# Kernel tuning notes

Measured on AMD Instinct MI355X. Metric: run time of the kernel, lower is better.

The kernel has to match this reference:

```python
import jax, jax.numpy as jnp
import numpy as np

TOTAL_WORDS = 90000
EMBED = 100
SEQ = 300
BATCH = 250
UNITS = 1024


def setup_inputs() -> dict:
    key = jax.random.key(0)
    ks = jax.random.split(key, 9)
    s = 0.02
    return {
        "tokens": jax.random.randint(ks[0], (BATCH, SEQ), 0, TOTAL_WORDS),
        "emb": jax.random.normal(ks[1], (TOTAL_WORDS, EMBED), jnp.float32) * s,
        "Wx0": jax.random.normal(ks[2], (EMBED, UNITS), jnp.float32) * s,
        "Wh0": jax.random.normal(ks[3], (UNITS, UNITS), jnp.float32) * s,
        "b0": jnp.zeros((UNITS,), jnp.float32),
        "Wx1": jax.random.normal(ks[4], (UNITS, UNITS), jnp.float32) * s,
        "Wh1": jax.random.normal(ks[5], (UNITS, UNITS), jnp.float32) * s,
        "b1": jnp.zeros((UNITS,), jnp.float32),
        "Wo": jax.random.normal(ks[6], (UNITS, 1), jnp.float32) * s,
        "bo": jnp.zeros((1,), jnp.float32),
    }


def reference(tokens, emb, Wx0, Wh0, b0, Wx1, Wh1, b1, Wo, bo):
    # Embedding lookup: [B, S, E]
    x = emb[tokens]
    # Precompute input projections for both cells' input-side matmuls where possible.
    # Cell0 input projection can be done for all timesteps at once: [B, S, U]
    xp0 = jnp.einsum("bse,eu->bsu", x, Wx0) + b0

    def step(carry, xp_t):
        h0, h1 = carry
        # SimpleRNNCell: out = tanh(x@Wx + h@Wh + b); dropout disabled (inference)
        h0 = jnp.tanh(xp_t + h0 @ Wh0)
        h1 = jnp.tanh(h0 @ Wx1 + h1 @ Wh1 + b1)
        return (h0, h1), None

    h0 = jnp.zeros((BATCH, UNITS), jnp.float32)
    h1 = jnp.zeros((BATCH, UNITS), jnp.float32)
    # scan over time: xp0 transposed to [S, B, U]
    (h0, h1), _ = jax.lax.scan(step, (h0, h1), jnp.transpose(xp0, (1, 0, 2)))
    logits = h1 @ Wo + bo  # [B, 1]
    return jax.nn.sigmoid(logits)
```

## Files before the change

kernel.cpp:

```cpp
#include <hip/hip_runtime.h>
#include <hip/hip_bf16.h>

#define SEQ 300
#define BAT 250
#define UNITS 1024
#define EMBD 100
#define MROWS (SEQ*BAT)

typedef __bf16 bf16;
typedef __bf16 bf16x4 __attribute__((ext_vector_type(4)));
typedef __bf16 bf16x8 __attribute__((ext_vector_type(8)));
typedef float  f32x2  __attribute__((ext_vector_type(2)));
typedef float  f32x4  __attribute__((ext_vector_type(4)));
typedef float  f32x16 __attribute__((ext_vector_type(16)));
typedef unsigned u32x4 __attribute__((ext_vector_type(4)));

#define MFMA32(a,b,c) __builtin_amdgcn_mfma_f32_32x32x16_bf16(a,b,c,0,0,0)
#define F32X16_ZERO {0.f,0.f,0.f,0.f,0.f,0.f,0.f,0.f,0.f,0.f,0.f,0.f,0.f,0.f,0.f,0.f}

__device__ __align__(16)  bf16 g_xp0[(size_t)MROWS*UNITS + 8192];
__device__ __align__(256) bf16 g_h0[304][256*1024];
__device__ __align__(256) bf16 g_h1[304][256*1024];
__device__ __align__(64) unsigned g_pf0[8*16];
__device__ __align__(64) unsigned g_pf1[8*16];

struct L16 { u32x4 a, b, c, d; };

#define ISSUE_LINE(L, P) \
  asm volatile("global_load_dwordx4 %0, %4, off sc0 sc1\n\t" \
               "global_load_dwordx4 %1, %4, off offset:16 sc0 sc1\n\t" \
               "global_load_dwordx4 %2, %4, off offset:32 sc0 sc1\n\t" \
               "global_load_dwordx4 %3, %4, off offset:48 sc0 sc1" \
    : "=&v"((L).a), "=&v"((L).b), "=&v"((L).c), "=&v"((L).d) : "v"(P) : "memory")
#define ISSUE8(A, B, P) \
  asm volatile("global_load_dwordx4 %0, %2, off sc0 sc1\n\t" \
               "global_load_dwordx4 %1, %2, off offset:16 sc0 sc1" \
    : "=&v"(A), "=&v"(B) : "v"(P) : "memory")

__device__ __forceinline__ unsigned min8(const u32x4& a, const u32x4& b) {
  unsigned m0 = a[0] < a[1] ? a[0] : a[1];
  unsigned m1 = a[2] < a[3] ? a[2] : a[3];
  unsigned m2 = b[0] < b[1] ? b[0] : b[1];
  unsigned m3 = b[2] < b[3] ? b[2] : b[3];
  m0 = m0 < m1 ? m0 : m1; m2 = m2 < m3 ? m2 : m3;
  return m0 < m2 ? m0 : m2;
}
__device__ __forceinline__ unsigned minline(const L16& L) {
  unsigned m0 = min8(L.a, L.b), m1 = min8(L.c, L.d);
  return m0 < m1 ? m0 : m1;
}
__device__ __forceinline__ float tanh_fast(float x) {
  float e = __expf(2.f * x);
  return 1.f - 2.f / (e + 1.f);
}

__global__ __launch_bounds__(256) void xp0_kernel(const int* __restrict__ tokens,
                                                  const float* __restrict__ emb,
                                                  const float* __restrict__ Wx0,
                                                  const float* __restrict__ b0) {
  __shared__ bf16 A[64 * 128];
  __shared__ int toks[64];
  const int mt = blockIdx.x;
  const int nt = blockIdx.y;
  const int tid = threadIdx.x, lane = tid & 63, wv = tid >> 6;

  if (tid < 64) {
    int R = mt * 64 + tid;
    int tok = 0;
    if (R < MROWS) { int s = R / 250; int b = R - s * 250; tok = tokens[b * SEQ + s]; }
    toks[tid] = tok;
  }
  __syncthreads();
  for (int idx = tid; idx < 64 * 128; idx += 256) {
    int r = idx >> 7, k = idx & 127;
    float v = (k < EMBD) ? emb[(size_t)toks[r] * EMBD + k] : 0.f;
    unsigned off = (unsigned)(r * 256 + k * 2);
    off ^= (unsigned)((r & 7) << 4);
    *(bf16*)((char*)A + off) = (bf16)v;
  }

  const int colb = nt * 256 + (wv << 6) + (lane & 31);
  bf16x8 Bf[2][8];
  #pragma unroll
  for (int nf = 0; nf < 2; ++nf) {
    #pragma unroll
    for (int kk = 0; kk < 8; ++kk) {
      const int kb = (kk << 4) + ((lane >> 5) << 3);
      bf16x8 f;
      #pragma unroll
      for (int j = 0; j < 8; ++j) {
        int k = kb + j;
        f[j] = (bf16)((k < EMBD) ? Wx0[(size_t)k * UNITS + colb + (nf << 5)] : 0.f);
      }
      Bf[nf][kk] = f;
    }
  }
  __syncthreads();

  f32x16 acc00 = F32X16_ZERO, acc01 = F32X16_ZERO, acc10 = F32X16_ZERO, acc11 = F32X16_ZERO;
  #pragma unroll
  for (int kk = 0; kk < 8; ++kk) {
    #pragma unroll
    for (int mf = 0; mf < 2; ++mf) {
      int row = (mf << 5) + (lane & 31);
      unsigned off = (unsigned)(row * 256 + ((kk << 4) + ((lane >> 5) << 3)) * 2);
      off ^= (unsigned)((row & 7) << 4);
      bf16x8 a = *(const bf16x8*)((const char*)A + off);
      if (mf == 0) { acc00 = MFMA32(a, Bf[0][kk], acc00); acc01 = MFMA32(a, Bf[1][kk], acc01); }
      else         { acc10 = MFMA32(a, Bf[0][kk], acc10); acc11 = MFMA32(a, Bf[1][kk], acc11); }
    }
  }

  const float bb0 = b0[colb], bb1 = b0[colb + 32];
  #pragma unroll
  for (int mf = 0; mf < 2; ++mf) {
    #pragma unroll
    for (int nf = 0; nf < 2; ++nf) {
      #pragma unroll
      for (int reg = 0; reg < 16; ++reg) {
        int r32 = (mf << 5) + ((lane >> 5) << 2) + (reg & 3) + ((reg >> 2) << 3);
        int R = mt * 64 + r32;
        if (R < MROWS) {
          float v = (mf == 0 ? (nf == 0 ? acc00[reg] : acc01[reg])
                             : (nf == 0 ? acc10[reg] : acc11[reg])) + (nf ? bb1 : bb0);
          g_xp0[(size_t)R * UNITS + nt * 256 + (wv << 6) + (nf << 5) + (lane & 31)] = (bf16)v;
        }
      }
    }
  }
}

#define WAITV(N) do { asm volatile("s_waitcnt vmcnt(" #N ")" ::: "memory"); \
                      __builtin_amdgcn_sched_barrier(0); } while (0)
#define LDG(I, P) do { const bf16* _p = (P); \
  asm volatile("global_load_dwordx4 %0, %4, off\n\t" \
               "global_load_dwordx4 %1, %4, off offset:1024\n\t" \
               "global_load_dwordx4 %2, %4, off offset:2048\n\t" \
               "global_load_dwordx4 %3, %4, off offset:3072" \
    : "=&v"(av[I]), "=&v"(av[I+1]), "=&v"(av[I+2]), "=&v"(av[I+3]) : "v"(_p)); } while (0)
#define MF4(K0) { _Pragma("unroll") \
  for (int kk = (K0); kk < (K0) + 4; ++kk) { \
    bf16x8 a_ = __builtin_bit_cast(bf16x8, av[kk]); \
    acc0 = MFMA32(a_, Bf[0][kk], acc0); \
    acc1 = MFMA32(a_, Bf[1][kk], acc1); } }

__global__ __launch_bounds__(512, 1) void rnn_persistent(const float* __restrict__ Wh0,
                                                         const float* __restrict__ Wx1,
                                                         const float* __restrict__ Wh1,
                                                         const float* __restrict__ b1) {
  const int bx = blockIdx.x;
  const int role = (bx >= 128) ? 0 : 1;
  const int m8 = bx & 7;
  const int n  = role ? (bx >> 3) : ((bx - 128) >> 3);
  const int tid = threadIdx.x;
  const int lane = tid & 63, w = tid >> 6;
  const int sub = w & 1, kq = w >> 1;

  __shared__ bf16 red[8][32][68];

  const float* W = role ? (sub ? Wh1 : Wx1) : Wh0;
  bf16x8 Bf[2][16];
  {
    const int colA = role ? (n * 64 + (lane & 31)) : (n * 128 + (sub << 6) + (lane & 31));
    const int kb = (kq << 8) + ((lane >> 5) << 3);
    #pragma unroll
    for (int nf = 0; nf < 2; ++nf)
      #pragma unroll
      for (int kk = 0; kk < 16; ++kk) {
        const float* s = W + (size_t)(kb + (kk << 4)) * UNITS + colA + (nf << 5);
        bf16x8 f;
        #pragma unroll
        for (int j = 0; j < 8; ++j) f[j] = (bf16)s[(size_t)j * UNITS];
        Bf[nf][kk] = f;
      }
  }

  const size_t abase = ((size_t)(m8 * 128 + kq * 32 + (lane >> 5))) * 256 + (size_t)(lane & 31) * 8;

  if (role == 0) {
    const int cb = tid >> 5, rp = tid & 31;
    const int csub = cb >> 3;
    const int idx = (((cb >> 2) & 1) << 4) + (rp & 3) + ((rp >> 3) << 2);
    const int entry = ((((rp >> 2) & 1)) << 5) + ((cb & 3) << 3);
    const size_t hsb = ((size_t)(m8 * 128 + n * 16 + cb)) * 256 + (size_t)rp * 8;

    for (int t = 0; t < SEQ; ++t) {
      bf16x8 xv;
      { const bf16* xp = &g_xp0[(size_t)(t * BAT + m8 * 32 + rp) * UNITS + n * 128 + (cb << 3)];
        asm volatile("global_load_dwordx4 %0, %1, off" : "=&v"(xv) : "v"(xp)); }
      if (tid == 0 && t >= 1) {
        for (;;) {
          u32x4 fa, fb;
          ISSUE8(fa, fb, &g_pf0[m8 * 16]);
          asm volatile("s_waitcnt vmcnt(0)" ::: "memory");
          __builtin_amdgcn_sched_barrier(0);
          if (min8(fa, fb) >= (unsigned)t) break;
          __builtin_amdgcn_s_sleep(1);
        }
      }
      __syncthreads();

      f32x16 acc0 = F32X16_ZERO, acc1 = F32X16_ZERO;
      if (t >= 1) {
        f32x4 av[16];
        const bf16* pn = g_h0[t - 1] + abase;
        LDG(0, pn); LDG(4, pn + 2048); LDG(8, pn + 4096); LDG(12, pn + 6144);
        WAITV(12); MF4(0)
        WAITV(8);  MF4(4)
        WAITV(4);  MF4(8)
        WAITV(0);  MF4(12)
      }
      {
        const int s0 = kq * 2 + sub;
        #pragma unroll
        for (int r = 0; r < 16; ++r) {
          red[s0][r][lane]      = (bf16)acc0[r];
          red[s0][16 + r][lane] = (bf16)acc1[r];
        }
      }
      __syncthreads();
      WAITV(0);
      bf16* hb = g_h0[t] + hsb;
      {
        float s[8];
        #pragma unroll
        for (int j = 0; j < 8; ++j) s[j] = (float)xv[j];
        #pragma unroll
        for (int k4 = 0; k4 < 4; ++k4) {
          bf16x8 v = *(const bf16x8*)&red[k4 * 2 + csub][idx][entry];
          #pragma unroll
          for (int j = 0; j < 8; ++j) s[j] += (float)v[j];
        }
        union { bf16 h[8]; f32x4 v; } o;
        #pragma unroll
        for (int j = 0; j < 8; ++j) o.h[j] = (bf16)tanh_fast(s[j]);
        asm volatile("global_store_dwordx4 %0, %1, off sc0 sc1" :: "v"(hb), "v"(o.v) : "memory");
      }
      asm volatile("s_waitcnt vmcnt(0)" ::: "memory");
      __syncthreads();
      if (tid == 0) {
        unsigned v = (unsigned)(t + 1);
        asm volatile("global_store_dword %0, %1, off sc0 sc1" :: "v"(&g_pf0[m8 * 16 + n]), "v"(v) : "memory");
      }
      { f32x4 d;
        asm volatile("global_load_dwordx4 %0, %1, off sc0 sc1" : "=&v"(d) : "v"(hb)); }
    }
  } else {
    const int rp = tid & 31, cg = tid >> 5;
    const int nfc = cg >> 3;
    const int entc = (((rp >> 2) & 1) << 5) + ((cg & 7) << 2);
    const int regc = (rp & 3) + ((rp >> 3) << 2);
    const size_t hsb = ((size_t)(m8 * 128 + n * 8 + (cg >> 1))) * 256 + (size_t)rp * 8 + (size_t)((cg & 1) << 2);
    float b1v[4];
    #pragma unroll
    for (int j = 0; j < 4; ++j) b1v[j] = b1[n * 64 + (cg << 2) + j];

    for (int t = 1; t <= SEQ; ++t) {
      if (tid == 0) {
        for (;;) {
          u32x4 fa, fb;
          ISSUE8(fa, fb, &g_pf0[m8 * 16]);
          asm volatile("s_waitcnt vmcnt(0)" ::: "memory");
          __builtin_amdgcn_sched_barrier(0);
          if (min8(fa, fb) >= (unsigned)t) break;
          __builtin_amdgcn_s_sleep(1);
        }
      }
      __syncthreads();

      f32x16 acc0 = F32X16_ZERO, acc1 = F32X16_ZERO;
      if (sub == 0) {
        f32x4 av[16];
        const bf16* pn = g_h0[t - 1] + abase;
        LDG(0, pn); LDG(4, pn + 2048); LDG(8, pn + 4096); LDG(12, pn + 6144);
        WAITV(12); MF4(0)
        WAITV(8);  MF4(4)
        WAITV(4);  MF4(8)
        WAITV(0);  MF4(12)
        const int s0 = kq * 2;
        #pragma unroll
        for (int r = 0; r < 16; ++r) {
          red[s0][r][lane]      = (bf16)acc0[r];
          red[s0][16 + r][lane] = (bf16)acc1[r];
        }
      } else if (tid == 64 && t >= 2) {
        for (;;) {
          L16 B;
          ISSUE_LINE(B, &g_pf1[m8 * 16]);
          asm volatile("s_waitcnt vmcnt(0)" ::: "memory");
          __builtin_amdgcn_sched_barrier(0);
          if (minline(B) >= (unsigned)(t - 1)) break;
          __builtin_amdgcn_s_sleep(1);
        }
      }
      __syncthreads();

      if (sub == 1) {
        if (t >= 2) {
          f32x4 av[16];
          const bf16* pn = g_h1[t - 1] + abase;
          LDG(0, pn); LDG(4, pn + 2048); LDG(8, pn + 4096); LDG(12, pn + 6144);
          WAITV(12); MF4(0)
          WAITV(8);  MF4(4)
          WAITV(4);  MF4(8)
          WAITV(0);  MF4(12)
        }
        const int s0 = kq * 2 + 1;
        #pragma unroll
        for (int r = 0; r < 16; ++r) {
          red[s0][r][lane]      = (bf16)acc0[r];
          red[s0][16 + r][lane] = (bf16)acc1[r];
        }
      }
      __syncthreads();

      bf16* hb = g_h1[t] + hsb;
      {
        float s[4];
        #pragma unroll
        for (int j = 0; j < 4; ++j) s[j] = b1v[j];
        #pragma unroll
        for (int w8 = 0; w8 < 8; ++w8) {
          bf16x4 v = *(const bf16x4*)&red[w8][(nfc << 4) + regc][entc];
          #pragma unroll
          for (int j = 0; j < 4; ++j) s[j] += (float)v[j];
        }
        union { bf16 h[4]; f32x2 v; } o;
        #pragma unroll
        for (int j = 0; j < 4; ++j) o.h[j] = (bf16)tanh_fast(s[j]);
        asm volatile("global_store_dwordx2 %0, %1, off sc0 sc1" :: "v"(hb), "v"(o.v) : "memory");
      }
      asm volatile("s_waitcnt vmcnt(0)" ::: "memory");
      __syncthreads();
      if (tid == 0) {
        unsigned v = (unsigned)t;
        asm volatile("global_store_dword %0, %1, off sc0 sc1" :: "v"(&g_pf1[m8 * 16 + n]), "v"(v) : "memory");
      }
      { f32x2 d;
        asm volatile("global_load_dwordx2 %0, %1, off sc0 sc1" : "=&v"(d) : "v"(hb)); }
    }
  }
}

__global__ __launch_bounds__(64) void logits_kernel(const float* __restrict__ Wo,
                                                    const float* __restrict__ bo,
                                                    float* __restrict__ out) {
  const int b = blockIdx.x, lane = threadIdx.x;
  if (b == 0) {
    unsigned z = 0;
    for (int i = lane; i < 256; i += 64) {
      unsigned* p = (i < 128) ? &g_pf0[i] : &g_pf1[i - 128];
      asm volatile("global_store_dword %0, %1, off sc0 sc1" :: "v"(p), "v"(z) : "memory");
    }
    asm volatile("s_waitcnt vmcnt(0)" ::: "memory");
  }
  const bf16* h = g_h1[SEQ];
  const size_t base = ((size_t)((b >> 5) * 128 + lane * 2)) * 256 + (size_t)(b & 31) * 8;
  bf16x8 v0 = *(const bf16x8*)&h[base];
  bf16x8 v1 = *(const bf16x8*)&h[base + 256];
  float s = 0.f;
  #pragma unroll
  for (int j = 0; j < 8; ++j) {
    s += (float)v0[j] * Wo[lane * 16 + j];
    s += (float)v1[j] * Wo[lane * 16 + 8 + j];
  }
  #pragma unroll
  for (int off = 32; off; off >>= 1) s += __shfl_xor(s, off, 64);
  if (lane == 0) out[b] = 1.f / (1.f + __expf(-(s + bo[0])));
}

extern "C" void kernel_launch(void* const* d_in, const int* in_sizes, int n_in,
                              void* d_out, int out_size, void* d_ws, size_t ws_size,
                              hipStream_t stream) {
  const int*   tokens = (const int*)  d_in[0];
  const float* emb    = (const float*)d_in[1];
  const float* Wx0    = (const float*)d_in[2];
  const float* Wh0    = (const float*)d_in[3];
  const float* b0     = (const float*)d_in[4];
  const float* Wx1    = (const float*)d_in[5];
  const float* Wh1    = (const float*)d_in[6];
  const float* b1     = (const float*)d_in[7];
  const float* Wo     = (const float*)d_in[8];
  const float* bo     = (const float*)d_in[9];
  float* out = (float*)d_out;

  dim3 gx((MROWS + 63) / 64, 4);
  xp0_kernel<<<gx, 256, 0, stream>>>(tokens, emb, Wx0, b0);

  rnn_persistent<<<192, 512, 0, stream>>>(Wh0, Wx1, Wh1, b1);

  logits_kernel<<<BAT, 64, 0, stream>>>(Wo, bo, out);
}
```

Before: 1.841 ms.

## Per-wave flag polling, drop block barriers, use release fence instead of write-through stores

Replaces the thread-0 spin plus __syncthreads at the start of each timestep with per-wave polling of the progress flags. Each wave now waits only on the dependency it actually needs, so in the layer-1 role the h0 and h1 waves proceed independently and one block barrier per step is removed. Hidden-state stores become ordinary stores, and visibility to other blocks is ensured by an agent-scope release fence before the flag store, which also replaces the old dummy read-back loads. The risks are more concurrent polling traffic, a longer sleep interval, and relying on the fence for correctness of cross-block visibility.

```diff
diff --git a/kernel.cpp b/kernel.cpp
--- a/kernel.cpp
+++ b/kernel.cpp
@@ -52,6 +52,34 @@
 __device__ __forceinline__ float tanh_fast(float x) {
   float e = __expf(2.f * x);
   return 1.f - 2.f / (e + 1.f);
+}
+__device__ __forceinline__ void poll8(const unsigned* line, unsigned target, int lane) {
+  if (lane == 0) {
+    for (;;) {
+      u32x4 fa, fb;
+      ISSUE8(fa, fb, line);
+      asm volatile("s_waitcnt vmcnt(0)" ::: "memory");
+      __builtin_amdgcn_sched_barrier(0);
+      if (min8(fa, fb) >= target) break;
+      __builtin_amdgcn_s_sleep(2);
+    }
+  }
+}
+__device__ __forceinline__ void poll16(const unsigned* line, unsigned target, int lane) {
+  if (lane == 0) {
+    for (;;) {
+      L16 B;
+      ISSUE_LINE(B, line);
+      asm volatile("s_waitcnt vmcnt(0)" ::: "memory");
+      __builtin_amdgcn_sched_barrier(0);
+      if (minline(B) >= target) break;
+      __builtin_amdgcn_s_sleep(2);
+    }
+  }
+}
+__device__ __forceinline__ void release_to_mall() {
+  __builtin_amdgcn_fence(__ATOMIC_RELEASE, "agent");
+  asm volatile("s_waitcnt vmcnt(0)" ::: "memory");
 }
 
 __global__ __launch_bounds__(256) void xp0_kernel(const int* __restrict__ tokens,
@@ -188,17 +216,7 @@
       bf16x8 xv;
       { const bf16* xp = &g_xp0[(size_t)(t * BAT + m8 * 32 + rp) * UNITS + n * 128 + (cb << 3)];
         asm volatile("global_load_dwordx4 %0, %1, off" : "=&v"(xv) : "v"(xp)); }
-      if (tid == 0 && t >= 1) {
-        for (;;) {
-          u32x4 fa, fb;
-          ISSUE8(fa, fb, &g_pf0[m8 * 16]);
-          asm volatile("s_waitcnt vmcnt(0)" ::: "memory");
-          __builtin_amdgcn_sched_barrier(0);
-          if (min8(fa, fb) >= (unsigned)t) break;
-          __builtin_amdgcn_s_sleep(1);
-        }
-      }
-      __syncthreads();
+      if (t >= 1) poll8(&g_pf0[m8 * 16], (unsigned)t, lane);
 
       f32x16 acc0 = F32X16_ZERO, acc1 = F32X16_ZERO;
       if (t >= 1) {
@@ -234,16 +252,15 @@
         union { bf16 h[8]; f32x4 v; } o;
         #pragma unroll
         for (int j = 0; j < 8; ++j) o.h[j] = (bf16)tanh_fast(s[j]);
-        asm volatile("global_store_dwordx4 %0, %1, off sc0 sc1" :: "v"(hb), "v"(o.v) : "memory");
+        asm volatile("global_store_dwordx4 %0, %1, off" :: "v"(hb), "v"(o.v) : "memory");
       }
       asm volatile("s_waitcnt vmcnt(0)" ::: "memory");
       __syncthreads();
       if (tid == 0) {
+        release_to_mall();
         unsigned v = (unsigned)(t + 1);
         asm volatile("global_store_dword %0, %1, off sc0 sc1" :: "v"(&g_pf0[m8 * 16 + n]), "v"(v) : "memory");
       }
-      { f32x4 d;
-        asm volatile("global_load_dwordx4 %0, %1, off sc0 sc1" : "=&v"(d) : "v"(hb)); }
     }
   } else {
     const int rp = tid & 31, cg = tid >> 5;
@@ -256,20 +273,9 @@
     for (int j = 0; j < 4; ++j) b1v[j] = b1[n * 64 + (cg << 2) + j];
 
     for (int t = 1; t <= SEQ; ++t) {
-      if (tid == 0) {
-        for (;;) {
-          u32x4 fa, fb;
-          ISSUE8(fa, fb, &g_pf0[m8 * 16]);
-          asm volatile("s_waitcnt vmcnt(0)" ::: "memory");
-          __builtin_amdgcn_sched_barrier(0);
-          if (min8(fa, fb) >= (unsigned)t) break;
-          __builtin_amdgcn_s_sleep(1);
-        }
-      }
-      __syncthreads();
-
       f32x16 acc0 = F32X16_ZERO, acc1 = F32X16_ZERO;
       if (sub == 0) {
+        poll8(&g_pf0[m8 * 16], (unsigned)t, lane);
         f32x4 av[16];
         const bf16* pn = g_h0[t - 1] + abase;
         LDG(0, pn); LDG(4, pn + 2048); LDG(8, pn + 4096); LDG(12, pn + 6144);
@@ -277,35 +283,18 @@
         WAITV(8);  MF4(4)
         WAITV(4);  MF4(8)
         WAITV(0);  MF4(12)
-        const int s0 = kq * 2;
-        #pragma unroll
-        for (int r = 0; r < 16; ++r) {
-          red[s0][r][lane]      = (bf16)acc0[r];
-          red[s0][16 + r][lane] = (bf16)acc1[r];
-        }
-      } else if (tid == 64 && t >= 2) {
-        for (;;) {
-          L16 B;
-          ISSUE_LINE(B, &g_pf1[m8 * 16]);
-          asm volatile("s_waitcnt vmcnt(0)" ::: "memory");
-          __builtin_amdgcn_sched_barrier(0);
-          if (minline(B) >= (unsigned)(t - 1)) break;
-          __builtin_amdgcn_s_sleep(1);
-        }
-      }
-      __syncthreads();
-
-      if (sub == 1) {
-        if (t >= 2) {
-          f32x4 av[16];
-          const bf16* pn = g_h1[t - 1] + abase;
-          LDG(0, pn); LDG(4, pn + 2048); LDG(8, pn + 4096); LDG(12, pn + 6144);
-          WAITV(12); MF4(0)
-          WAITV(8);  MF4(4)
-          WAITV(4);  MF4(8)
-          WAITV(0);  MF4(12)
-        }
-        const int s0 = kq * 2 + 1;
+      } else if (t >= 2) {
+        poll16(&g_pf1[m8 * 16], (unsigned)(t - 1), lane);
+        f32x4 av[16];
+        const bf16* pn = g_h1[t - 1] + abase;
+        LDG(0, pn); LDG(4, pn + 2048); LDG(8, pn + 4096); LDG(12, pn + 6144);
+        WAITV(12); MF4(0)
+        WAITV(8);  MF4(4)
+        WAITV(4);  MF4(8)
+        WAITV(0);  MF4(12)
+      }
+      {
+        const int s0 = kq * 2 + sub;
         #pragma unroll
         for (int r = 0; r < 16; ++r) {
           red[s0][r][lane]      = (bf16)acc0[r];
@@ -328,16 +317,15 @@
         union { bf16 h[4]; f32x2 v; } o;
         #pragma unroll
         for (int j = 0; j < 4; ++j) o.h[j] = (bf16)tanh_fast(s[j]);
-        asm volatile("global_store_dwordx2 %0, %1, off sc0 sc1" :: "v"(hb), "v"(o.v) : "memory");
+        asm volatile("global_store_dwordx2 %0, %1, off" :: "v"(hb), "v"(o.v) : "memory");
       }
       asm volatile("s_waitcnt vmcnt(0)" ::: "memory");
       __syncthreads();
       if (tid == 0) {
+        release_to_mall();
         unsigned v = (unsigned)t;
         asm volatile("global_store_dword %0, %1, off sc0 sc1" :: "v"(&g_pf1[m8 * 16 + n]), "v"(v) : "memory");
       }
-      { f32x2 d;
-        asm volatile("global_load_dwordx2 %0, %1, off sc0 sc1" : "=&v"(d) : "v"(hb)); }
     }
   }
 }
```

Measured after the change: 3.483 ms. +89.1%, slower.

## Replace layer-1 block barriers with per-wave LDS gate flags

Applied to the files above, without the earlier changes.

In the layer-1 role, the two global flag polls (layer-0 readiness and layer-1 previous-step readiness) now publish to workgroup-scope LDS gate variables. Each wave spins only on the gate it needs, so the Wx1 and Wh1 sub-waves can run their matmuls concurrently instead of in sequence behind two __syncthreads. The dummy global reload of the just-stored hidden state is also removed in both roles. This saves one block barrier per step and lets the two halves overlap, at the risk of weaker ordering: only lane 0 spins, the other lanes rely on implicit wave convergence, and dropping the reload may change global visibility timing.

```diff
diff --git a/kernel.cpp b/kernel.cpp
--- a/kernel.cpp
+++ b/kernel.cpp
@@ -52,6 +52,15 @@
 __device__ __forceinline__ float tanh_fast(float x) {
   float e = __expf(2.f * x);
   return 1.f - 2.f / (e + 1.f);
+}
+__device__ __forceinline__ void lds_post(unsigned* p, unsigned v) {
+  __hip_atomic_store(p, v, __ATOMIC_RELEASE, __HIP_MEMORY_SCOPE_WORKGROUP);
+}
+__device__ __forceinline__ void lds_spin(unsigned* p, unsigned target, int lane) {
+  if (lane == 0) {
+    while (__hip_atomic_load(p, __ATOMIC_ACQUIRE, __HIP_MEMORY_SCOPE_WORKGROUP) < target)
+      __builtin_amdgcn_s_sleep(1);
+  }
 }
 
 __global__ __launch_bounds__(256) void xp0_kernel(const int* __restrict__ tokens,
@@ -157,6 +166,7 @@
   const int sub = w & 1, kq = w >> 1;
 
   __shared__ bf16 red[8][32][68];
+  __shared__ unsigned shm_gate[2];
 
   const float* W = role ? (sub ? Wh1 : Wx1) : Wh0;
   bf16x8 Bf[2][16];
@@ -242,8 +252,6 @@
         unsigned v = (unsigned)(t + 1);
         asm volatile("global_store_dword %0, %1, off sc0 sc1" :: "v"(&g_pf0[m8 * 16 + n]), "v"(v) : "memory");
       }
-      { f32x4 d;
-        asm volatile("global_load_dwordx4 %0, %1, off sc0 sc1" : "=&v"(d) : "v"(hb)); }
     }
   } else {
     const int rp = tid & 31, cg = tid >> 5;
@@ -254,6 +262,9 @@
     float b1v[4];
     #pragma unroll
     for (int j = 0; j < 4; ++j) b1v[j] = b1[n * 64 + (cg << 2) + j];
+
+    if (tid < 2) shm_gate[tid] = 0;
+    __syncthreads();
 
     for (int t = 1; t <= SEQ; ++t) {
       if (tid == 0) {
@@ -265,11 +276,23 @@
           if (min8(fa, fb) >= (unsigned)t) break;
           __builtin_amdgcn_s_sleep(1);
         }
-      }
-      __syncthreads();
+        lds_post(&shm_gate[0], (unsigned)t);
+      }
+      if (tid == 64 && t >= 2) {
+        for (;;) {
+          L16 B;
+          ISSUE_LINE(B, &g_pf1[m8 * 16]);
+          asm volatile("s_waitcnt vmcnt(0)" ::: "memory");
+          __builtin_amdgcn_sched_barrier(0);
+          if (minline(B) >= (unsigned)(t - 1)) break;
+          __builtin_amdgcn_s_sleep(1);
+        }
+        lds_post(&shm_gate[1], (unsigned)(t - 1));
+      }
 
       f32x16 acc0 = F32X16_ZERO, acc1 = F32X16_ZERO;
       if (sub == 0) {
+        lds_spin(&shm_gate[0], (unsigned)t, lane);
         f32x4 av[16];
         const bf16* pn = g_h0[t - 1] + abase;
         LDG(0, pn); LDG(4, pn + 2048); LDG(8, pn + 4096); LDG(12, pn + 6144);
@@ -277,35 +300,18 @@
         WAITV(8);  MF4(4)
         WAITV(4);  MF4(8)
         WAITV(0);  MF4(12)
-        const int s0 = kq * 2;
-        #pragma unroll
-        for (int r = 0; r < 16; ++r) {
-          red[s0][r][lane]      = (bf16)acc0[r];
-          red[s0][16 + r][lane] = (bf16)acc1[r];
-        }
-      } else if (tid == 64 && t >= 2) {
-        for (;;) {
-          L16 B;
-          ISSUE_LINE(B, &g_pf1[m8 * 16]);
-          asm volatile("s_waitcnt vmcnt(0)" ::: "memory");
-          __builtin_amdgcn_sched_barrier(0);
-          if (minline(B) >= (unsigned)(t - 1)) break;
-          __builtin_amdgcn_s_sleep(1);
-        }
-      }
-      __syncthreads();
-
-      if (sub == 1) {
-        if (t >= 2) {
-          f32x4 av[16];
-          const bf16* pn = g_h1[t - 1] + abase;
-          LDG(0, pn); LDG(4, pn + 2048); LDG(8, pn + 4096); LDG(12, pn + 6144);
-          WAITV(12); MF4(0)
-          WAITV(8);  MF4(4)
-          WAITV(4);  MF4(8)
-          WAITV(0);  MF4(12)
-        }
-        const int s0 = kq * 2 + 1;
+      } else if (t >= 2) {
+        lds_spin(&shm_gate[1], (unsigned)(t - 1), lane);
+        f32x4 av[16];
+        const bf16* pn = g_h1[t - 1] + abase;
+        LDG(0, pn); LDG(4, pn + 2048); LDG(8, pn + 4096); LDG(12, pn + 6144);
+        WAITV(12); MF4(0)
+        WAITV(8);  MF4(4)
+        WAITV(4);  MF4(8)
+        WAITV(0);  MF4(12)
+      }
+      {
+        const int s0 = kq * 2 + sub;
         #pragma unroll
         for (int r = 0; r < 16; ++r) {
           red[s0][r][lane]      = (bf16)acc0[r];
@@ -336,8 +342,6 @@
         unsigned v = (unsigned)t;
         asm volatile("global_store_dword %0, %1, off sc0 sc1" :: "v"(&g_pf1[m8 * 16 + n]), "v"(v) : "memory");
       }
-      { f32x2 d;
-        asm volatile("global_load_dwordx2 %0, %1, off sc0 sc1" : "=&v"(d) : "v"(hb)); }
     }
   }
 }
```

New measurement: 1.942 ms. +5.5%, slower.
